# Performance work log

Hardware: AMD Instinct MI355X
Metric: run time of the kernel (lower is better)

Reference implementation:

```python
import jax, jax.numpy as jnp
import numpy as np


def setup_inputs() -> dict:
    key = jax.random.key(0)
    ks = jax.random.split(key, 8)
    B, S, Nc, C, Cseed = 4, 4096, 8192, 512, 256
    return {
        "query_xyz": jax.random.normal(ks[0], (B, S, 3), dtype=jnp.float32),
        "ref_xyz": jax.random.normal(ks[1], (B, Nc, 3), dtype=jnp.float32),
        "ref_feat": jax.random.normal(ks[2], (B, C, Nc), dtype=jnp.float32),
        "seed_features": jax.random.normal(ks[3], (B, Cseed, S), dtype=jnp.float32),
        "W_seed_proj": jax.random.normal(ks[4], (Cseed, C), dtype=jnp.float32) * 0.02,
        "b_seed_proj": jax.random.normal(ks[5], (Cseed,), dtype=jnp.float32) * 0.02,
        "W_concat_proj": jax.random.normal(ks[6], (Cseed, 2 * Cseed), dtype=jnp.float32) * 0.02,
        "b_concat_proj": jax.random.normal(ks[7], (Cseed,), dtype=jnp.float32) * 0.02,
    }


def _nn_gather(query_xyz, ref_xyz, ref_feat):
    # torch.cdist(p=2) + argmin: argmin over squared distance is identical
    # (sqrt is monotonic), so we skip the sqrt.
    q2 = jnp.sum(query_xyz * query_xyz, axis=-1, keepdims=True)      # (B,S,1)
    r2 = jnp.sum(ref_xyz * ref_xyz, axis=-1)[:, None, :]             # (B,1,Nc)
    qr = jnp.einsum("bsd,bnd->bsn", query_xyz, ref_xyz)              # (B,S,Nc)
    d2 = q2 + r2 - 2.0 * qr                                          # (B,S,Nc)
    idx = jnp.argmin(d2, axis=-1)                                    # (B,S) int
    # gather nearest-neighbor features: (B,C,Nc) -> (B,C,S)
    return jnp.take_along_axis(ref_feat, idx[:, None, :], axis=2)


def reference(query_xyz, ref_xyz, ref_feat, seed_features,
              W_seed_proj, b_seed_proj, W_concat_proj, b_concat_proj):
    lift3d_raw = _nn_gather(query_xyz, ref_xyz, ref_feat)            # (B,C,S)
    # 1x1 Conv1d == channel matmul
    lift3d_seed = jnp.einsum("oc,bcs->bos", W_seed_proj, lift3d_raw) \
                  + b_seed_proj[None, :, None]                       # (B,256,S)
    fused = jnp.concatenate([seed_features, lift3d_seed], axis=1)    # (B,512,S)
    out = jnp.einsum("oc,bcs->bos", W_concat_proj, fused) \
          + b_concat_proj[None, :, None]                             # (B,256,S)
    return out
```

## Files before the change

### kernel.cpp

```cpp
#include <hip/hip_runtime.h>

#define B_   4
#define S_   4096
#define NC   8192
#define C_   512
#define CS   256
#define KTOT 768
#define NPAIR 4096

typedef __attribute__((ext_vector_type(8))) short short8;
typedef __attribute__((ext_vector_type(4))) float f32x4;
typedef float v2f __attribute__((ext_vector_type(2)));

static __device__ __forceinline__ unsigned short f2bf(float x) {
    unsigned u = __builtin_bit_cast(unsigned, x);
    unsigned r = u + 0x7FFFu + ((u >> 16) & 1u);
    return (unsigned short)(r >> 16);
}

static __device__ __forceinline__ v2f pk_mul(v2f a, v2f b) {
    v2f d;
    asm("v_pk_mul_f32 %0, %1, %2" : "=v"(d) : "v"(a), "v"(b));
    return d;
}
static __device__ __forceinline__ v2f pk_add(v2f a, v2f b) {
    v2f d;
    asm("v_pk_add_f32 %0, %1, %2" : "=v"(d) : "v"(a), "v"(b));
    return d;
}
static __device__ __forceinline__ v2f pk_sub(v2f a, v2f b) {
    v2f d;
    asm("v_pk_add_f32 %0, %1, %2 neg_lo:[0,1] neg_hi:[0,1]" : "=v"(d) : "v"(a), "v"(b));
    return d;
}

__global__ __launch_bounds__(256) void pad_ref_kernel(const float* __restrict__ rxyz,
                                                      float4* __restrict__ refpk) {
    int gid = blockIdx.x * 256 + threadIdx.x;
    int b = gid >> 12;
    int pr = gid & 4095;
    const float* p0 = rxyz + ((size_t)b * NC + pr * 2) * 3;
    float x0 = p0[0], y0 = p0[1], z0 = p0[2];
    float x1 = p0[3], y1 = p0[4], z1 = p0[5];
    float r20 = __fadd_rn(__fadd_rn(__fmul_rn(x0, x0), __fmul_rn(y0, y0)), __fmul_rn(z0, z0));
    float r21 = __fadd_rn(__fadd_rn(__fmul_rn(x1, x1), __fmul_rn(y1, y1)), __fmul_rn(z1, z1));
    refpk[gid]                = make_float4(x0, x1, y0, y1);
    refpk[B_ * NPAIR + gid]   = make_float4(z0, z1, r20, r21);
}

__global__ __launch_bounds__(256) void argmin_kernel(const float* __restrict__ qxyz,
                                                     const float4* __restrict__ refpk,
                                                     int* __restrict__ idxout) {
    int tid = threadIdx.x;
    int lane = tid & 63;
    int qg = tid >> 6;
    int b = blockIdx.y;
    int sbase = blockIdx.x * 32 + qg * 8;

    v2f qx2[8], qy2[8], qz2[8], q22[8];
    #pragma unroll
    for (int q = 0; q < 8; ++q) {
        const float* qp = qxyz + ((size_t)(b * S_ + sbase + q)) * 3;
        float qx = qp[0], qy = qp[1], qz = qp[2];
        float q2 = __fadd_rn(__fadd_rn(__fmul_rn(qx, qx), __fmul_rn(qy, qy)),
                             __fmul_rn(qz, qz));
        qx2[q] = (v2f){qx, qx};
        qy2[q] = (v2f){qy, qy};
        qz2[q] = (v2f){qz, qz};
        q22[q] = (v2f){q2, q2};
    }

    const float4* p1 = refpk + (size_t)b * NPAIR + lane;
    const float4* p2 = p1 + (size_t)B_ * NPAIR;

    float be[8], bo[8];
    int pe[8], po[8];
    #pragma unroll
    for (int q = 0; q < 8; ++q) {
        be[q] = 3.4028235e38f; bo[q] = 3.4028235e38f; pe[q] = 0; po[q] = 0;
    }

    #pragma unroll 2
    for (int j = 0; j < 64; ++j) {
        float4 v1 = p1[j * 64];
        float4 v2 = p2[j * 64];
        v2f xs = {v1.x, v1.y}, ys = {v1.z, v1.w};
        v2f zs = {v2.x, v2.y}, ws = {v2.z, v2.w};
        #pragma unroll
        for (int q = 0; q < 8; ++q) {
            v2f qr = pk_add(pk_add(pk_mul(qx2[q], xs), pk_mul(qy2[q], ys)),
                            pk_mul(qz2[q], zs));
            v2f d2 = pk_sub(pk_add(q22[q], ws), pk_add(qr, qr));
            if (d2.x < be[q]) { be[q] = d2.x; pe[q] = j; }
            if (d2.y < bo[q]) { bo[q] = d2.y; po[q] = j; }
        }
    }

    __shared__ float sval[32][64];
    __shared__ int   sidx[32][64];
    #pragma unroll
    for (int q = 0; q < 8; ++q) {
        int ie = ((pe[q] * 64 + lane) << 1);
        int io = ((po[q] * 64 + lane) << 1) | 1;
        float bv; int bx;
        if (bo[q] < be[q] || (bo[q] == be[q] && io < ie)) { bv = bo[q]; bx = io; }
        else                                              { bv = be[q]; bx = ie; }
        sval[qg * 8 + q][lane] = bv;
        sidx[qg * 8 + q][lane] = bx;
    }
    __syncthreads();
    if (tid < 32) {
        float v = sval[tid][0];
        int x = sidx[tid][0];
        #pragma unroll 8
        for (int l = 1; l < 64; ++l) {
            float vv = sval[tid][l];
            int xx = sidx[tid][l];
            if (vv < v || (vv == v && xx < x)) { v = vv; x = xx; }
        }
        idxout[b * S_ + blockIdx.x * 32 + tid] = x;
    }
}

__global__ __launch_bounds__(256) void transpose_kernel(const float* __restrict__ rf,
                                                        unsigned short* __restrict__ refT) {
    __shared__ float t[64][65];
    int tid = threadIdx.x;
    int b = blockIdx.z;
    int c0 = blockIdx.y * 64;
    int n0 = blockIdx.x * 64;
    int tx = tid & 15, ty = tid >> 4;
    #pragma unroll
    for (int r = 0; r < 4; ++r) {
        int c = r * 16 + ty;
        float4 v = *(const float4*)(rf + ((size_t)b * C_ + c0 + c) * NC + n0 + tx * 4);
        t[tx * 4 + 0][c] = v.x;
        t[tx * 4 + 1][c] = v.y;
        t[tx * 4 + 2][c] = v.z;
        t[tx * 4 + 3][c] = v.w;
    }
    __syncthreads();
    #pragma unroll
    for (int r = 0; r < 4; ++r) {
        int n = r * 16 + ty;
        ushort4 o;
        o.x = f2bf(t[n][tx * 4 + 0]);
        o.y = f2bf(t[n][tx * 4 + 1]);
        o.z = f2bf(t[n][tx * 4 + 2]);
        o.w = f2bf(t[n][tx * 4 + 3]);
        *(ushort4*)(refT + ((size_t)b * NC + n0 + n) * C_ + c0 + tx * 4) = o;
    }
}

__global__ __launch_bounds__(256) void wc_kernel(const float* __restrict__ Wcat,
                                                 const float* __restrict__ Wseed,
                                                 unsigned short* __restrict__ Wcomb) {
    __shared__ float sa[64][68];
    __shared__ float sbt[64][68];
    int tid = threadIdx.x;
    int to = blockIdx.y * 64;
    int tc = blockIdx.x * 64;
    int tx = tid & 15, ty = tid >> 4;
    float acc[4][4] = {};
    for (int kt = 0; kt < 256; kt += 64) {
        __syncthreads();
        #pragma unroll
        for (int r = 0; r < 4; ++r) {
            int oo = r * 16 + ty;
            float4 v = *(const float4*)(Wcat + (size_t)(to + oo) * 512 + 256 + kt + tx * 4);
            sa[oo][tx * 4 + 0] = v.x;
            sa[oo][tx * 4 + 1] = v.y;
            sa[oo][tx * 4 + 2] = v.z;
            sa[oo][tx * 4 + 3] = v.w;
            float4 u = *(const float4*)(Wseed + (size_t)(kt + oo) * 512 + tc + tx * 4);
            sbt[oo][tx * 4 + 0] = u.x;
            sbt[oo][tx * 4 + 1] = u.y;
            sbt[oo][tx * 4 + 2] = u.z;
            sbt[oo][tx * 4 + 3] = u.w;
        }
        __syncthreads();
        for (int k = 0; k < 64; ++k) {
            float a[4], bb[4];
            #pragma unroll
            for (int i = 0; i < 4; ++i) a[i] = sa[ty * 4 + i][k];
            #pragma unroll
            for (int j = 0; j < 4; ++j) bb[j] = sbt[k][tx * 4 + j];
            #pragma unroll
            for (int i = 0; i < 4; ++i)
                #pragma unroll
                for (int j = 0; j < 4; ++j)
                    acc[i][j] = fmaf(a[i], bb[j], acc[i][j]);
        }
    }
    #pragma unroll
    for (int i = 0; i < 4; ++i)
        #pragma unroll
        for (int j = 0; j < 4; ++j)
            Wcomb[(size_t)(to + ty * 4 + i) * KTOT + 256 + tc + tx * 4 + j] = f2bf(acc[i][j]);
}

__global__ __launch_bounds__(256) void w1_kernel(const float* __restrict__ Wcat,
                                                 unsigned short* __restrict__ Wcomb) {
    int gid = blockIdx.x * 256 + threadIdx.x;
    int o = gid >> 8, c = gid & 255;
    Wcomb[(size_t)o * KTOT + c] = f2bf(Wcat[(size_t)o * 512 + c]);
}

__global__ __launch_bounds__(256) void beff_kernel(const float* __restrict__ Wcat,
                                                   const float* __restrict__ bseed,
                                                   const float* __restrict__ bcat,
                                                   float* __restrict__ beff) {
    int o = threadIdx.x;
    float acc = bcat[o];
    const float4* wp = (const float4*)(Wcat + (size_t)o * 512 + 256);
    const float4* bp = (const float4*)bseed;
    #pragma unroll 4
    for (int j = 0; j < 64; ++j) {
        float4 w = wp[j];
        float4 bb = bp[j];
        acc = fmaf(w.x, bb.x, acc);
        acc = fmaf(w.y, bb.y, acc);
        acc = fmaf(w.z, bb.z, acc);
        acc = fmaf(w.w, bb.w, acc);
    }
    beff[o] = acc;
}

__global__ __launch_bounds__(256) void fused_gemm_kernel(
        const unsigned short* __restrict__ Wcomb,
        const float* __restrict__ seed,
        const unsigned short* __restrict__ refT,
        const int* __restrict__ idx,
        const float* __restrict__ beff,
        float* __restrict__ out) {
    __shared__ __align__(16) unsigned short sA[128][72];
    __shared__ __align__(16) unsigned short sB[32][72];
    __shared__ int sIdx[32];
    __shared__ float sBias[128];

    int tid = threadIdx.x;
    int b = blockIdx.z;
    int m0 = blockIdx.y * 128;
    int s0 = blockIdx.x * 32;
    if (tid < 32) sIdx[tid] = idx[b * S_ + s0 + tid];
    if (tid < 128) sBias[tid] = beff[m0 + tid];

    int lane = tid & 63;
    int w = tid >> 6;
    int ln = lane & 15;
    int quad = lane >> 4;
    int q8 = quad * 8;

    f32x4 acc[2][2];
    #pragma unroll
    for (int i = 0; i < 2; ++i)
        #pragma unroll
        for (int j = 0; j < 2; ++j)
            acc[i][j] = (f32x4){0.f, 0.f, 0.f, 0.f};

    for (int ks = 0; ks < 12; ++ks) {
        int k0 = ks * 64;
        __syncthreads();
        #pragma unroll
        for (int i = 0; i < 4; ++i) {
            int ch = tid + 256 * i;
            int mm = ch >> 3;
            int kk8 = (ch & 7) << 3;
            *(short8*)&sA[mm][kk8] =
                *(const short8*)(Wcomb + (size_t)(m0 + mm) * KTOT + k0 + kk8);
        }
        if (k0 < 256) {
            int n = tid & 31;
            int kk8 = (tid >> 5) << 3;
            const float* sp = seed + ((size_t)b * CS + k0 + kk8) * S_ + s0 + n;
            unsigned short tmp[8];
            #pragma unroll
            for (int r = 0; r < 8; ++r)
                tmp[r] = f2bf(sp[(size_t)r * S_]);
            *(short8*)&sB[n][kk8] = *(const short8*)tmp;
        } else {
            int n = tid >> 3;
            int kk8 = (tid & 7) << 3;
            const unsigned short* gp =
                refT + ((size_t)b * NC + sIdx[n]) * C_ + (k0 - 256) + kk8;
            *(short8*)&sB[n][kk8] = *(const short8*)gp;
        }
        __syncthreads();
        #pragma unroll
        for (int kf = 0; kf < 2; ++kf) {
            short8 af[2], bfr[2];
            #pragma unroll
            for (int i = 0; i < 2; ++i)
                af[i] = *(const short8*)&sA[w * 32 + i * 16 + ln][kf * 32 + q8];
            #pragma unroll
            for (int j = 0; j < 2; ++j)
                bfr[j] = *(const short8*)&sB[j * 16 + ln][kf * 32 + q8];
            #pragma unroll
            for (int i = 0; i < 2; ++i)
                #pragma unroll
                for (int j = 0; j < 2; ++j)
                    acc[i][j] = __builtin_amdgcn_mfma_f32_16x16x32_bf16(af[i], bfr[j], acc[i][j], 0, 0, 0);
        }
    }

    #pragma unroll
    for (int i = 0; i < 2; ++i) {
        int mb = w * 32 + i * 16 + quad * 4;
        #pragma unroll
        for (int j = 0; j < 2; ++j) {
            int col = s0 + j * 16 + ln;
            #pragma unroll
            for (int r = 0; r < 4; ++r) {
                int m = mb + r;
                out[((size_t)b * CS + m0 + m) * S_ + col] = acc[i][j][r] + sBias[m];
            }
        }
    }
}

extern "C" void kernel_launch(void* const* d_in, const int* in_sizes, int n_in,
                              void* d_out, int out_size, void* d_ws, size_t ws_size,
                              hipStream_t stream) {
    const float* qxyz  = (const float*)d_in[0];
    const float* rxyz  = (const float*)d_in[1];
    const float* rfeat = (const float*)d_in[2];
    const float* seed  = (const float*)d_in[3];
    const float* Wseed = (const float*)d_in[4];
    const float* bseed = (const float*)d_in[5];
    const float* Wcat  = (const float*)d_in[6];
    const float* bcat  = (const float*)d_in[7];
    float* out = (float*)d_out;

    char* ws = (char*)d_ws;
    float4* refpk         = (float4*)(ws);
    int* idxbuf           = (int*)(ws + 1048576);
    float* beff           = (float*)(ws + 1114112);
    unsigned short* Wcomb = (unsigned short*)(ws + 1115136);
    unsigned short* refT  = (unsigned short*)(ws + 1508352);

    hipLaunchKernelGGL(pad_ref_kernel,    dim3(64),          dim3(256), 0, stream, rxyz, refpk);
    hipLaunchKernelGGL(argmin_kernel,     dim3(128, 4),      dim3(256), 0, stream, qxyz, refpk, idxbuf);
    hipLaunchKernelGGL(transpose_kernel,  dim3(128, 8, 4),   dim3(256), 0, stream, rfeat, refT);
    hipLaunchKernelGGL(wc_kernel,         dim3(8, 4),        dim3(256), 0, stream, Wcat, Wseed, Wcomb);
    hipLaunchKernelGGL(w1_kernel,         dim3(256),         dim3(256), 0, stream, Wcat, Wcomb);
    hipLaunchKernelGGL(beff_kernel,       dim3(1),           dim3(256), 0, stream, Wcat, bseed, bcat, beff);
    hipLaunchKernelGGL(fused_gemm_kernel, dim3(128, 2, 4),   dim3(256), 0, stream,
                       Wcomb, seed, refT, idxbuf, beff, out);
}
```

Before: 221.9 us.

## Split argmin over reference chunks and merge partials in GEMM prologue

Drops the reference-packing kernel and has the argmin kernel read raw xyz directly, computing |r|^2 inline. The reference set is split into 4 chunks along a new grid dimension, giving 4x more blocks to fill the GPU. Each block writes a per-chunk partial min and index, and the fused GEMM merges the four partials when loading its gather indices. This trades some extra per-point arithmetic and strided 3-float loads for higher occupancy, one fewer launch, and no separate reduction pass. The shared-memory reduction arrays are also laid out with padding to avoid bank conflicts.

```diff
diff --git a/kernel.cpp b/kernel.cpp
--- a/kernel.cpp
+++ b/kernel.cpp
@@ -6,7 +6,6 @@
 #define C_   512
 #define CS   256
 #define KTOT 768
-#define NPAIR 4096
 
 typedef __attribute__((ext_vector_type(8))) short short8;
 typedef __attribute__((ext_vector_type(4))) float f32x4;
@@ -34,28 +33,16 @@
     return d;
 }
 
-__global__ __launch_bounds__(256) void pad_ref_kernel(const float* __restrict__ rxyz,
-                                                      float4* __restrict__ refpk) {
-    int gid = blockIdx.x * 256 + threadIdx.x;
-    int b = gid >> 12;
-    int pr = gid & 4095;
-    const float* p0 = rxyz + ((size_t)b * NC + pr * 2) * 3;
-    float x0 = p0[0], y0 = p0[1], z0 = p0[2];
-    float x1 = p0[3], y1 = p0[4], z1 = p0[5];
-    float r20 = __fadd_rn(__fadd_rn(__fmul_rn(x0, x0), __fmul_rn(y0, y0)), __fmul_rn(z0, z0));
-    float r21 = __fadd_rn(__fadd_rn(__fmul_rn(x1, x1), __fmul_rn(y1, y1)), __fmul_rn(z1, z1));
-    refpk[gid]                = make_float4(x0, x1, y0, y1);
-    refpk[B_ * NPAIR + gid]   = make_float4(z0, z1, r20, r21);
-}
-
-__global__ __launch_bounds__(256) void argmin_kernel(const float* __restrict__ qxyz,
-                                                     const float4* __restrict__ refpk,
-                                                     int* __restrict__ idxout) {
+__global__ __launch_bounds__(256) void argmin_partial_kernel(
+        const float* __restrict__ qxyz, const float* __restrict__ rxyz,
+        float* __restrict__ pval, int* __restrict__ pidx) {
     int tid = threadIdx.x;
     int lane = tid & 63;
     int qg = tid >> 6;
-    int b = blockIdx.y;
-    int sbase = blockIdx.x * 32 + qg * 8;
+    int sblk = blockIdx.x;
+    int c = blockIdx.y;
+    int b = blockIdx.z;
+    int sbase = sblk * 32 + qg * 8;
 
     v2f qx2[8], qy2[8], qz2[8], q22[8];
     #pragma unroll
@@ -70,9 +57,7 @@
         q22[q] = (v2f){q2, q2};
     }
 
-    const float4* p1 = refpk + (size_t)b * NPAIR + lane;
-    const float4* p2 = p1 + (size_t)B_ * NPAIR;
-
+    const float* rp = rxyz + ((size_t)b * NC + 2 * (c * 1024 + lane)) * 3;
     float be[8], bo[8];
     int pe[8], po[8];
     #pragma unroll
@@ -80,12 +65,14 @@
         be[q] = 3.4028235e38f; bo[q] = 3.4028235e38f; pe[q] = 0; po[q] = 0;
     }
 
-    #pragma unroll 2
-    for (int j = 0; j < 64; ++j) {
-        float4 v1 = p1[j * 64];
-        float4 v2 = p2[j * 64];
-        v2f xs = {v1.x, v1.y}, ys = {v1.z, v1.w};
-        v2f zs = {v2.x, v2.y}, ws = {v2.z, v2.w};
+    #pragma unroll 4
+    for (int j = 0; j < 16; ++j) {
+        const float* jp = rp + j * 384;
+        float2 v1 = *(const float2*)(jp + 0);
+        float2 v2 = *(const float2*)(jp + 2);
+        float2 v3 = *(const float2*)(jp + 4);
+        v2f xs = {v1.x, v2.y}, ys = {v1.y, v3.x}, zs = {v2.x, v3.y};
+        v2f ws = pk_add(pk_add(pk_mul(xs, xs), pk_mul(ys, ys)), pk_mul(zs, zs));
         #pragma unroll
         for (int q = 0; q < 8; ++q) {
             v2f qr = pk_add(pk_add(pk_mul(qx2[q], xs), pk_mul(qy2[q], ys)),
@@ -96,29 +83,31 @@
         }
     }
 
-    __shared__ float sval[32][64];
-    __shared__ int   sidx[32][64];
+    __shared__ float sv[64][33];
+    __shared__ int   sx[64][33];
     #pragma unroll
     for (int q = 0; q < 8; ++q) {
-        int ie = ((pe[q] * 64 + lane) << 1);
-        int io = ((po[q] * 64 + lane) << 1) | 1;
+        int ie = (c * 1024 + pe[q] * 64 + lane) * 2;
+        int io = (c * 1024 + po[q] * 64 + lane) * 2 + 1;
         float bv; int bx;
         if (bo[q] < be[q] || (bo[q] == be[q] && io < ie)) { bv = bo[q]; bx = io; }
         else                                              { bv = be[q]; bx = ie; }
-        sval[qg * 8 + q][lane] = bv;
-        sidx[qg * 8 + q][lane] = bx;
+        sv[lane][qg * 8 + q] = bv;
+        sx[lane][qg * 8 + q] = bx;
     }
     __syncthreads();
     if (tid < 32) {
-        float v = sval[tid][0];
-        int x = sidx[tid][0];
+        float v = sv[0][tid];
+        int x = sx[0][tid];
         #pragma unroll 8
         for (int l = 1; l < 64; ++l) {
-            float vv = sval[tid][l];
-            int xx = sidx[tid][l];
+            float vv = sv[l][tid];
+            int xx = sx[l][tid];
             if (vv < v || (vv == v && xx < x)) { v = vv; x = xx; }
         }
-        idxout[b * S_ + blockIdx.x * 32 + tid] = x;
+        int qs = b * S_ + sblk * 32 + tid;
+        pval[qs * 4 + c] = v;
+        pidx[qs * 4 + c] = x;
     }
 }
 
@@ -230,7 +219,8 @@
         const unsigned short* __restrict__ Wcomb,
         const float* __restrict__ seed,
         const unsigned short* __restrict__ refT,
-        const int* __restrict__ idx,
+        const float* __restrict__ pval,
+        const int* __restrict__ pidx,
         const float* __restrict__ beff,
         float* __restrict__ out) {
     __shared__ __align__(16) unsigned short sA[128][72];
@@ -242,7 +232,18 @@
     int b = blockIdx.z;
     int m0 = blockIdx.y * 128;
     int s0 = blockIdx.x * 32;
-    if (tid < 32) sIdx[tid] = idx[b * S_ + s0 + tid];
+    if (tid < 32) {
+        int qs = b * S_ + s0 + tid;
+        float v = pval[qs * 4 + 0];
+        int x = pidx[qs * 4 + 0];
+        #pragma unroll
+        for (int c = 1; c < 4; ++c) {
+            float vv = pval[qs * 4 + c];
+            int xx = pidx[qs * 4 + c];
+            if (vv < v || (vv == v && xx < x)) { v = vv; x = xx; }
+        }
+        sIdx[tid] = x & (NC - 1);
+    }
     if (tid < 128) sBias[tid] = beff[m0 + tid];
 
     int lane = tid & 63;
@@ -332,18 +333,18 @@
     float* out = (float*)d_out;
 
     char* ws = (char*)d_ws;
-    float4* refpk         = (float4*)(ws);
-    int* idxbuf           = (int*)(ws + 1048576);
-    float* beff           = (float*)(ws + 1114112);
-    unsigned short* Wcomb = (unsigned short*)(ws + 1115136);
-    unsigned short* refT  = (unsigned short*)(ws + 1508352);
-
-    hipLaunchKernelGGL(pad_ref_kernel,    dim3(64),          dim3(256), 0, stream, rxyz, refpk);
-    hipLaunchKernelGGL(argmin_kernel,     dim3(128, 4),      dim3(256), 0, stream, qxyz, refpk, idxbuf);
-    hipLaunchKernelGGL(transpose_kernel,  dim3(128, 8, 4),   dim3(256), 0, stream, rfeat, refT);
-    hipLaunchKernelGGL(wc_kernel,         dim3(8, 4),        dim3(256), 0, stream, Wcat, Wseed, Wcomb);
-    hipLaunchKernelGGL(w1_kernel,         dim3(256),         dim3(256), 0, stream, Wcat, Wcomb);
-    hipLaunchKernelGGL(beff_kernel,       dim3(1),           dim3(256), 0, stream, Wcat, bseed, bcat, beff);
-    hipLaunchKernelGGL(fused_gemm_kernel, dim3(128, 2, 4),   dim3(256), 0, stream,
-                       Wcomb, seed, refT, idxbuf, beff, out);
-}
+    float* pval           = (float*)(ws);
+    int* pidx             = (int*)(ws + 262144);
+    float* beff           = (float*)(ws + 524288);
+    unsigned short* Wcomb = (unsigned short*)(ws + 525312);
+    unsigned short* refT  = (unsigned short*)(ws + 1048576);
+
+    hipLaunchKernelGGL(argmin_partial_kernel, dim3(128, 4, 4), dim3(256), 0, stream,
+                       qxyz, rxyz, pval, pidx);
+    hipLaunchKernelGGL(transpose_kernel,      dim3(128, 8, 4), dim3(256), 0, stream, rfeat, refT);
+    hipLaunchKernelGGL(wc_kernel,             dim3(8, 4),      dim3(256), 0, stream, Wcat, Wseed, Wcomb);
+    hipLaunchKernelGGL(w1_kernel,             dim3(256),       dim3(256), 0, stream, Wcat, Wcomb);
+    hipLaunchKernelGGL(beff_kernel,           dim3(1),         dim3(256), 0, stream, Wcat, bseed, bcat, beff);
+    hipLaunchKernelGGL(fused_gemm_kernel,     dim3(128, 2, 4), dim3(256), 0, stream,
+                       Wcomb, seed, refT, pval, pidx, beff, out);
+}
```

After: 223.7 us. About the same (+0.8%).
